# Performance work log

Measured on AMD Instinct MI355X. Metric: run time of the kernel, lower is better.

The kernel has to match this reference:

```python
import jax, jax.numpy as jnp
import numpy as np

N_NODES = 100000
N_EDGES = 300000
HID = 256
N0, N1, N2 = 40000, 30000, 30000
D0, D1, D2 = 512, 256, 128


def setup_inputs() -> dict:
    key = jax.random.key(0)
    ks = jax.random.split(key, 14)
    s = 0.05  # init scale
    return {
        "feat0": jax.random.normal(ks[0], (N0, D0), jnp.float32),
        "feat1": jax.random.normal(ks[1], (N1, D1), jnp.float32),
        "feat2": jax.random.normal(ks[2], (N2, D2), jnp.float32),
        # per-type Linear(in_dim, HID) params (torch Linear: y = x @ W.T + b)
        "fc_w0": jax.random.normal(ks[3], (HID, D0), jnp.float32) * s,
        "fc_b0": jnp.zeros((HID,), jnp.float32),
        "fc_w1": jax.random.normal(ks[4], (HID, D1), jnp.float32) * s,
        "fc_b1": jnp.zeros((HID,), jnp.float32),
        "fc_w2": jax.random.normal(ks[5], (HID, D2), jnp.float32) * s,
        "fc_b2": jnp.zeros((HID,), jnp.float32),
        # GraphConv 1: weight=False, bias=True
        "gc1_bias": jnp.zeros((HID,), jnp.float32),
        # GraphConv 2: weight (in,out) + bias (DGL convention: feat @ W)
        "gc2_weight": jax.random.normal(ks[6], (HID, HID), jnp.float32) * s,
        "gc2_bias": jnp.zeros((HID,), jnp.float32),
        "semantic_weight": jax.random.normal(ks[7], (1, 5), jnp.float32),
        "src": jax.random.randint(ks[8], (N_EDGES,), 0, N_NODES, jnp.int64),
        "dst": jax.random.randint(ks[9], (N_EDGES,), 0, N_NODES, jnp.int64),
    }


def reference(feat0, feat1, feat2, fc_w0, fc_b0, fc_w1, fc_b1, fc_w2, fc_b2,
              gc1_bias, gc2_weight, gc2_bias, semantic_weight, src, dst):
    # per-type projection then concat along node dim -> [N_NODES, HID]
    h = jnp.concatenate([
        feat0 @ fc_w0.T + fc_b0,
        feat1 @ fc_w1.T + fc_b1,
        feat2 @ fc_w2.T + fc_b2,
    ], axis=0)

    ones = jnp.ones((src.shape[0],), h.dtype)
    deg_out = jnp.maximum(jax.ops.segment_sum(ones, src, num_segments=N_NODES), 1.0)
    deg_in = jnp.maximum(jax.ops.segment_sum(ones, dst, num_segments=N_NODES), 1.0)
    norm_out = jax.lax.rsqrt(deg_out)[:, None]  # D_out^{-1/2}
    norm_in = jax.lax.rsqrt(deg_in)[:, None]    # D_in^{-1/2}

    def gconv(x, W, b):
        # DGL GraphConv, norm='both': D_in^{-1/2} A D_out^{-1/2} x W + b, relu
        msg = (x * norm_out)[src]                                  # [E, HID]
        agg = jax.ops.segment_sum(msg, dst, num_segments=N_NODES)  # [N, HID]
        agg = agg * norm_in
        if W is not None:
            agg = agg @ W
        return jax.nn.relu(agg + b)

    # dropout is identity in eval mode
    h = gconv(h, None, gc1_bias)        # layer 0: weight=False
    h = gconv(h, gc2_weight, gc2_bias)  # layer 1
    return h, semantic_weight
```

## Files before the change

### kernel.cpp

```cpp
#include <hip/hip_runtime.h>
#include <cstdint>

#define HID 256
static constexpr int    NNODES = 100000;
static constexpr int    NEDGES = 300000;
static constexpr size_t NH     = (size_t)NNODES * HID;
static constexpr int    SCAN_B = 256;
static constexpr int    NSBLK  = (NNODES + SCAN_B - 1) / SCAN_B;

typedef __attribute__((ext_vector_type(8))) short bf16x8;
typedef __attribute__((ext_vector_type(4))) float f32x4;

__device__ __forceinline__ unsigned short f2bf(float x) {
    unsigned int u = __float_as_uint(x);
    u += 0x7fffu + ((u >> 16) & 1u);
    return (unsigned short)(u >> 16);
}
__device__ __forceinline__ float bflo(unsigned int u) { return __uint_as_float(u << 16); }
__device__ __forceinline__ float bfhi(unsigned int u) { return __uint_as_float(u & 0xffff0000u); }

__global__ void zero_i32_k(int* __restrict__ p, int n) {
    int i = blockIdx.x * blockDim.x + threadIdx.x;
    if (i < n) p[i] = 0;
}

__global__ void cvt_bf16_k(const float* __restrict__ in, unsigned short* __restrict__ o, int n4) {
    int i = blockIdx.x * blockDim.x + threadIdx.x;
    if (i < n4) {
        float4 v = ((const float4*)in)[i];
        ushort4 w;
        w.x = f2bf(v.x); w.y = f2bf(v.y); w.z = f2bf(v.z); w.w = f2bf(v.w);
        ((ushort4*)o)[i] = w;
    }
}

__global__ void cvt_w2T_k(const float* __restrict__ w, unsigned short* __restrict__ o) {
    int n = blockIdx.x, k = threadIdx.x;
    o[n * 256 + k] = f2bf(w[k * 256 + n]);
}

__global__ void count_deg_k(const int* __restrict__ src, const int* __restrict__ dst,
                            int* __restrict__ degout, int* __restrict__ degin) {
    int e = blockIdx.x * blockDim.x + threadIdx.x;
    if (e < NEDGES) {
        atomicAdd(degout + src[e], 1);
        atomicAdd(degin  + dst[e], 1);
    }
}

__global__ void finalize_norm_k(const int* __restrict__ degout, const int* __restrict__ degin,
                                float* __restrict__ nout, float* __restrict__ nin,
                                const float* __restrict__ sw, float* __restrict__ tail) {
    int i = blockIdx.x * blockDim.x + threadIdx.x;
    if (i < NNODES) {
        nout[i] = rsqrtf(fmaxf((float)degout[i], 1.0f));
        nin[i]  = rsqrtf(fmaxf((float)degin[i], 1.0f));
    }
    if (i < 5) tail[i] = sw[i];
}

__global__ void scan_a_k(const int* __restrict__ degin, int* __restrict__ row_off,
                         int* __restrict__ bsums) {
    __shared__ int sm[SCAN_B];
    int t = threadIdx.x;
    int g = blockIdx.x * SCAN_B + t;
    int v = (g < NNODES) ? degin[g] : 0;
    sm[t] = v;
    __syncthreads();
#pragma unroll
    for (int off = 1; off < SCAN_B; off <<= 1) {
        int x = (t >= off) ? sm[t - off] : 0;
        __syncthreads();
        sm[t] += x;
        __syncthreads();
    }
    if (g < NNODES) row_off[g] = sm[t] - v;
    if (t == SCAN_B - 1) bsums[blockIdx.x] = sm[t];
}

__global__ void scan_b_k(int* __restrict__ bsums) {
    __shared__ int sm[512];
    int t = threadIdx.x;
    int v = (t < NSBLK) ? bsums[t] : 0;
    sm[t] = v;
    __syncthreads();
#pragma unroll
    for (int off = 1; off < 512; off <<= 1) {
        int x = (t >= off) ? sm[t - off] : 0;
        __syncthreads();
        sm[t] += x;
        __syncthreads();
    }
    if (t < NSBLK) bsums[t] = sm[t] - v;
}

__global__ void scan_c_k(int* __restrict__ row_off, const int* __restrict__ bsums) {
    int g = blockIdx.x * SCAN_B + threadIdx.x;
    if (g < NNODES) row_off[g] += bsums[blockIdx.x];
    if (g == 0) row_off[NNODES] = NEDGES;
}

__global__ void fill_csr_k(const int* __restrict__ src, const int* __restrict__ dst,
                           const int* __restrict__ row_off, int* __restrict__ cursor,
                           int* __restrict__ csr_src) {
    int e = blockIdx.x * blockDim.x + threadIdx.x;
    if (e < NEDGES) {
        int d = dst[e];
        int pos = row_off[d] + atomicAdd(cursor + d, 1);
        csr_src[pos] = src[e];
    }
}

template <int EPI>
__global__ __launch_bounds__(256) void gather_bf16_k(
    const unsigned short* __restrict__ h, const int* __restrict__ row_off,
    const int* __restrict__ csr_src, const float* __restrict__ nin,
    const float* __restrict__ nout, const float* __restrict__ bias,
    unsigned short* __restrict__ out)
{
    int node = blockIdx.x * 4 + (threadIdx.x >> 6);
    if (node >= NNODES) return;
    int lane = threadIdx.x & 63;
    int beg = row_off[node], end = row_off[node + 1];
    float a0 = 0.f, a1 = 0.f, a2 = 0.f, a3 = 0.f;
    for (int e = beg; e < end; ++e) {
        int s = csr_src[e];
        uint2 v = *(const uint2*)(h + (size_t)s * HID + lane * 4);
        a0 += bflo(v.x); a1 += bfhi(v.x);
        a2 += bflo(v.y); a3 += bfhi(v.y);
    }
    if (EPI) {
        float ni = nin[node], no = nout[node];
        float4 bb = *(const float4*)(bias + lane * 4);
        a0 = fmaxf(fmaf(a0, ni, bb.x), 0.f) * no;
        a1 = fmaxf(fmaf(a1, ni, bb.y), 0.f) * no;
        a2 = fmaxf(fmaf(a2, ni, bb.z), 0.f) * no;
        a3 = fmaxf(fmaf(a3, ni, bb.w), 0.f) * no;
    }
    ushort4 o;
    o.x = f2bf(a0); o.y = f2bf(a1); o.z = f2bf(a2); o.w = f2bf(a3);
    *(ushort4*)(out + (size_t)node * HID + lane * 4) = o;
}

template <int EPI>
__global__ __launch_bounds__(256) void mfma_gemm_k(
    const unsigned short* __restrict__ A, const unsigned short* __restrict__ Bn,
    const float* __restrict__ bias, const float* __restrict__ rs,
    void* __restrict__ Cv, int M, int K)
{
    __shared__ unsigned short As[128 * 32];
    __shared__ unsigned short Bs[128 * 32];
    const int tid  = threadIdx.x;
    const int wave = tid >> 6;
    const int lane = tid & 63;
    const int wm   = wave >> 1;
    const int wn   = wave & 1;
    const int m0   = blockIdx.x * 128;
    const int n0   = blockIdx.y * 128;

    f32x4 acc[4][4];
#pragma unroll
    for (int i = 0; i < 4; ++i)
#pragma unroll
        for (int j = 0; j < 4; ++j)
#pragma unroll
            for (int r = 0; r < 4; ++r) acc[i][j][r] = 0.f;

    const int half = lane >> 4;
    const int l15  = lane & 15;

    for (int k0 = 0; k0 < K; k0 += 32) {
#pragma unroll
        for (int t = 0; t < 2; ++t) {
            int q   = tid + t * 256;
            int row = q >> 2, c = q & 3;
            int slot = (c ^ ((row >> 1) & 3));
            int gm  = m0 + row; if (gm > M - 1) gm = M - 1;
            uint4 v = *(const uint4*)(A + (size_t)gm * K + k0 + c * 8);
            *(uint4*)&As[(row * 4 + slot) * 8] = v;
        }
#pragma unroll
        for (int t = 0; t < 2; ++t) {
            int q   = tid + t * 256;
            int row = q >> 2, c = q & 3;
            int slot = (c ^ ((row >> 1) & 3));
            uint4 v = *(const uint4*)(Bn + (size_t)(n0 + row) * K + k0 + c * 8);
            *(uint4*)&Bs[(row * 4 + slot) * 8] = v;
        }
        __syncthreads();

        bf16x8 af[4], bfr[4];
#pragma unroll
        for (int i = 0; i < 4; ++i) {
            int m = wm * 64 + i * 16 + l15;
            int ca = half ^ ((m >> 1) & 3);
            af[i] = *(const bf16x8*)&As[(m * 4 + ca) * 8];
            int n = wn * 64 + i * 16 + l15;
            int cb = half ^ ((n >> 1) & 3);
            bfr[i] = *(const bf16x8*)&Bs[(n * 4 + cb) * 8];
        }
#pragma unroll
        for (int i = 0; i < 4; ++i)
#pragma unroll
            for (int j = 0; j < 4; ++j)
                acc[i][j] = __builtin_amdgcn_mfma_f32_16x16x32_bf16(
                    af[i], bfr[j], acc[i][j], 0, 0, 0);
        __syncthreads();
    }

    float bj[4];
#pragma unroll
    for (int j = 0; j < 4; ++j) bj[j] = bias[n0 + wn * 64 + j * 16 + l15];

#pragma unroll
    for (int i = 0; i < 4; ++i)
#pragma unroll
        for (int r = 0; r < 4; ++r) {
            int m = m0 + wm * 64 + i * 16 + (lane >> 4) * 4 + r;
            if (m >= M) continue;
            float rsm = rs[m];
#pragma unroll
            for (int j = 0; j < 4; ++j) {
                int n = n0 + wn * 64 + j * 16 + l15;
                float v = acc[i][j][r];
                if (EPI == 0) {
                    v = (v + bj[j]) * rsm;
                    ((unsigned short*)Cv)[(size_t)m * HID + n] = f2bf(v);
                } else {
                    v = fmaxf(fmaf(v, rsm, bj[j]), 0.f);
                    ((float*)Cv)[(size_t)m * HID + n] = v;
                }
            }
        }
}

extern "C" void kernel_launch(void* const* d_in, const int* in_sizes, int n_in,
                              void* d_out, int out_size, void* d_ws, size_t ws_size,
                              hipStream_t stream)
{
    const float* feat0    = (const float*)d_in[0];
    const float* feat1    = (const float*)d_in[1];
    const float* feat2    = (const float*)d_in[2];
    const float* fc_w0    = (const float*)d_in[3];
    const float* fc_b0    = (const float*)d_in[4];
    const float* fc_w1    = (const float*)d_in[5];
    const float* fc_b1    = (const float*)d_in[6];
    const float* fc_w2    = (const float*)d_in[7];
    const float* fc_b2    = (const float*)d_in[8];
    const float* gc1_bias = (const float*)d_in[9];
    const float* gc2_w    = (const float*)d_in[10];
    const float* gc2_bias = (const float*)d_in[11];
    const float* sw       = (const float*)d_in[12];
    const int*   src      = (const int*)d_in[13];
    const int*   dst      = (const int*)d_in[14];

    char* base = (char*)d_ws;
    unsigned short* h0b   = (unsigned short*)base;
    unsigned short* h1b   = h0b + NH;
    unsigned short* agg2b = h0b;
    unsigned short* f0b   = h1b + NH;
    unsigned short* f1b   = f0b + (size_t)40000 * 512;
    unsigned short* f2b   = f1b + (size_t)30000 * 256;
    unsigned short* w0b   = f2b + (size_t)30000 * 128;
    unsigned short* w1b   = w0b + 256 * 512;
    unsigned short* w2b   = w1b + 256 * 256;
    unsigned short* w2Tb  = w2b + 256 * 128;
    float* nout = (float*)(w2Tb + 256 * 256 + 64);
    float* nin  = nout + NNODES;
    int* deg_out = (int*)(nin + NNODES);
    int* deg_in  = deg_out + NNODES;
    int* cursor  = deg_in + NNODES;
    int* row_off = cursor + NNODES;
    int* bsums   = row_off + NNODES + 1;
    int* csr_src = bsums + 512;
    float* out   = (float*)d_out;

    zero_i32_k<<<(3 * NNODES + 255) / 256, 256, 0, stream>>>(deg_out, 3 * NNODES);
    count_deg_k<<<(NEDGES + 255) / 256, 256, 0, stream>>>(src, dst, deg_out, deg_in);
    finalize_norm_k<<<(NNODES + 255) / 256, 256, 0, stream>>>(deg_out, deg_in, nout, nin,
                                                              sw, out + NH);
    scan_a_k<<<NSBLK, SCAN_B, 0, stream>>>(deg_in, row_off, bsums);
    scan_b_k<<<1, 512, 0, stream>>>(bsums);
    scan_c_k<<<NSBLK, SCAN_B, 0, stream>>>(row_off, bsums);
    fill_csr_k<<<(NEDGES + 255) / 256, 256, 0, stream>>>(src, dst, row_off, cursor, csr_src);

    cvt_bf16_k<<<(40000 * 512 / 4 + 255) / 256, 256, 0, stream>>>(feat0, f0b, 40000 * 512 / 4);
    cvt_bf16_k<<<(30000 * 256 / 4 + 255) / 256, 256, 0, stream>>>(feat1, f1b, 30000 * 256 / 4);
    cvt_bf16_k<<<(30000 * 128 / 4 + 255) / 256, 256, 0, stream>>>(feat2, f2b, 30000 * 128 / 4);
    cvt_bf16_k<<<(256 * 512 / 4 + 255) / 256, 256, 0, stream>>>(fc_w0, w0b, 256 * 512 / 4);
    cvt_bf16_k<<<(256 * 256 / 4 + 255) / 256, 256, 0, stream>>>(fc_w1, w1b, 256 * 256 / 4);
    cvt_bf16_k<<<(256 * 128 / 4 + 255) / 256, 256, 0, stream>>>(fc_w2, w2b, 256 * 128 / 4);
    cvt_w2T_k<<<256, 256, 0, stream>>>(gc2_w, w2Tb);

    mfma_gemm_k<0><<<dim3((40000 + 127) / 128, 2), 256, 0, stream>>>(
        f0b, w0b, fc_b0, nout, h0b, 40000, 512);
    mfma_gemm_k<0><<<dim3((30000 + 127) / 128, 2), 256, 0, stream>>>(
        f1b, w1b, fc_b1, nout + 40000, h0b + (size_t)40000 * HID, 30000, 256);
    mfma_gemm_k<0><<<dim3((30000 + 127) / 128, 2), 256, 0, stream>>>(
        f2b, w2b, fc_b2, nout + 70000, h0b + (size_t)70000 * HID, 30000, 128);

    gather_bf16_k<1><<<(NNODES + 3) / 4, 256, 0, stream>>>(h0b, row_off, csr_src,
                                                           nin, nout, gc1_bias, h1b);
    gather_bf16_k<0><<<(NNODES + 3) / 4, 256, 0, stream>>>(h1b, row_off, csr_src,
                                                           nin, nout, nullptr, agg2b);
    mfma_gemm_k<1><<<dim3((100000 + 127) / 128, 2), 256, 0, stream>>>(
        agg2b, w2Tb, gc2_bias, nin, out, 100000, 256);
}
```

Before: 464.9 us.

## Fuse bf16 conversion into projection GEMM and gather into final GEMM

Feature fp32-to-bf16 conversion moves into a single merged projection GEMM, which tiles 64 rows by the full 256 output columns and covers all three node types in one launch. The second-layer gather is fused into the final GEMM's prologue, staging aggregated rows straight into shared memory. Weight conversions and norm finalization are merged into existing kernels to cut launches and intermediate global traffic. The costs are higher LDS use per block and a gather phase that runs before any MFMA work in the final kernel.

```diff
diff --git a/kernel.cpp b/kernel.cpp
--- a/kernel.cpp
+++ b/kernel.cpp
@@ -16,27 +16,15 @@
     u += 0x7fffu + ((u >> 16) & 1u);
     return (unsigned short)(u >> 16);
 }
+__device__ __forceinline__ unsigned int pack2(float a, float b) {
+    return (unsigned int)f2bf(a) | ((unsigned int)f2bf(b) << 16);
+}
 __device__ __forceinline__ float bflo(unsigned int u) { return __uint_as_float(u << 16); }
 __device__ __forceinline__ float bfhi(unsigned int u) { return __uint_as_float(u & 0xffff0000u); }
 
 __global__ void zero_i32_k(int* __restrict__ p, int n) {
     int i = blockIdx.x * blockDim.x + threadIdx.x;
     if (i < n) p[i] = 0;
-}
-
-__global__ void cvt_bf16_k(const float* __restrict__ in, unsigned short* __restrict__ o, int n4) {
-    int i = blockIdx.x * blockDim.x + threadIdx.x;
-    if (i < n4) {
-        float4 v = ((const float4*)in)[i];
-        ushort4 w;
-        w.x = f2bf(v.x); w.y = f2bf(v.y); w.z = f2bf(v.z); w.w = f2bf(v.w);
-        ((ushort4*)o)[i] = w;
-    }
-}
-
-__global__ void cvt_w2T_k(const float* __restrict__ w, unsigned short* __restrict__ o) {
-    int n = blockIdx.x, k = threadIdx.x;
-    o[n * 256 + k] = f2bf(w[k * 256 + n]);
 }
 
 __global__ void count_deg_k(const int* __restrict__ src, const int* __restrict__ dst,
@@ -48,24 +36,40 @@
     }
 }
 
-__global__ void finalize_norm_k(const int* __restrict__ degout, const int* __restrict__ degin,
-                                float* __restrict__ nout, float* __restrict__ nin,
-                                const float* __restrict__ sw, float* __restrict__ tail) {
-    int i = blockIdx.x * blockDim.x + threadIdx.x;
-    if (i < NNODES) {
-        nout[i] = rsqrtf(fmaxf((float)degout[i], 1.0f));
-        nin[i]  = rsqrtf(fmaxf((float)degin[i], 1.0f));
-    }
-    if (i < 5) tail[i] = sw[i];
-}
-
-__global__ void scan_a_k(const int* __restrict__ degin, int* __restrict__ row_off,
-                         int* __restrict__ bsums) {
+__global__ void cvt_weights_k(const float* __restrict__ w0, const float* __restrict__ w1,
+                              const float* __restrict__ w2, const float* __restrict__ wg,
+                              unsigned short* __restrict__ o0, unsigned short* __restrict__ o1,
+                              unsigned short* __restrict__ o2, unsigned short* __restrict__ ogT) {
+    int b = blockIdx.x, t = threadIdx.x;
+    const float* in; unsigned short* out; int i;
+    if (b < 128)      { in = w0; out = o0; i = b * 256 + t; }
+    else if (b < 192) { in = w1; out = o1; i = (b - 128) * 256 + t; }
+    else if (b < 224) { in = w2; out = o2; i = (b - 192) * 256 + t; }
+    else {
+        int n = b - 224, k = t;
+        ogT[n * 256 + k] = f2bf(wg[k * 256 + n]);
+        return;
+    }
+    float4 v = ((const float4*)in)[i];
+    ushort4 w;
+    w.x = f2bf(v.x); w.y = f2bf(v.y); w.z = f2bf(v.z); w.w = f2bf(v.w);
+    ((ushort4*)out)[i] = w;
+}
+
+__global__ void scan_a_k(const int* __restrict__ degin, const int* __restrict__ degout,
+                         int* __restrict__ row_off, int* __restrict__ bsums,
+                         float* __restrict__ nout, float* __restrict__ nin,
+                         const float* __restrict__ sw, float* __restrict__ tail) {
     __shared__ int sm[SCAN_B];
     int t = threadIdx.x;
     int g = blockIdx.x * SCAN_B + t;
     int v = (g < NNODES) ? degin[g] : 0;
     sm[t] = v;
+    if (g < NNODES) {
+        nout[g] = rsqrtf(fmaxf((float)degout[g], 1.0f));
+        nin[g]  = rsqrtf(fmaxf((float)v, 1.0f));
+    }
+    if (g < 5) tail[g] = sw[g];
     __syncthreads();
 #pragma unroll
     for (int off = 1; off < SCAN_B; off <<= 1) {
@@ -111,7 +115,6 @@
     }
 }
 
-template <int EPI>
 __global__ __launch_bounds__(256) void gather_bf16_k(
     const unsigned short* __restrict__ h, const int* __restrict__ row_off,
     const int* __restrict__ csr_src, const float* __restrict__ nin,
@@ -129,62 +132,69 @@
         a0 += bflo(v.x); a1 += bfhi(v.x);
         a2 += bflo(v.y); a3 += bfhi(v.y);
     }
-    if (EPI) {
-        float ni = nin[node], no = nout[node];
-        float4 bb = *(const float4*)(bias + lane * 4);
-        a0 = fmaxf(fmaf(a0, ni, bb.x), 0.f) * no;
-        a1 = fmaxf(fmaf(a1, ni, bb.y), 0.f) * no;
-        a2 = fmaxf(fmaf(a2, ni, bb.z), 0.f) * no;
-        a3 = fmaxf(fmaf(a3, ni, bb.w), 0.f) * no;
-    }
+    float ni = nin[node], no = nout[node];
+    float4 bb = *(const float4*)(bias + lane * 4);
+    a0 = fmaxf(fmaf(a0, ni, bb.x), 0.f) * no;
+    a1 = fmaxf(fmaf(a1, ni, bb.y), 0.f) * no;
+    a2 = fmaxf(fmaf(a2, ni, bb.z), 0.f) * no;
+    a3 = fmaxf(fmaf(a3, ni, bb.w), 0.f) * no;
     ushort4 o;
     o.x = f2bf(a0); o.y = f2bf(a1); o.z = f2bf(a2); o.w = f2bf(a3);
     *(ushort4*)(out + (size_t)node * HID + lane * 4) = o;
 }
 
-template <int EPI>
-__global__ __launch_bounds__(256) void mfma_gemm_k(
-    const unsigned short* __restrict__ A, const unsigned short* __restrict__ Bn,
-    const float* __restrict__ bias, const float* __restrict__ rs,
-    void* __restrict__ Cv, int M, int K)
+__global__ __launch_bounds__(256, 3) void proj_mfma_k(
+    const float* __restrict__ f0, const float* __restrict__ f1, const float* __restrict__ f2,
+    const unsigned short* __restrict__ w0, const unsigned short* __restrict__ w1,
+    const unsigned short* __restrict__ w2,
+    const float* __restrict__ b0, const float* __restrict__ b1, const float* __restrict__ b2,
+    const float* __restrict__ nout, unsigned short* __restrict__ h0)
 {
-    __shared__ unsigned short As[128 * 32];
-    __shared__ unsigned short Bs[128 * 32];
+    __shared__ unsigned short As[64 * 32];
+    __shared__ unsigned short Bs[256 * 32];
+
+    int bx = blockIdx.x;
+    const float* A; const unsigned short* B; const float* bias; const float* rs;
+    unsigned short* C; int M, K;
+    if (bx < 625)       { A = f0; B = w0; bias = b0; rs = nout;          C = h0;                          M = 40000; K = 512; }
+    else if (bx < 1094) { bx -= 625;  A = f1; B = w1; bias = b1; rs = nout + 40000; C = h0 + (size_t)40000 * HID; M = 30000; K = 256; }
+    else                { bx -= 1094; A = f2; B = w2; bias = b2; rs = nout + 70000; C = h0 + (size_t)70000 * HID; M = 30000; K = 128; }
+    const int m0 = bx * 64;
+
     const int tid  = threadIdx.x;
-    const int wave = tid >> 6;
+    const int wn   = tid >> 6;
     const int lane = tid & 63;
-    const int wm   = wave >> 1;
-    const int wn   = wave & 1;
-    const int m0   = blockIdx.x * 128;
-    const int n0   = blockIdx.y * 128;
-
-    f32x4 acc[4][4];
-#pragma unroll
-    for (int i = 0; i < 4; ++i)
-#pragma unroll
-        for (int j = 0; j < 4; ++j)
-#pragma unroll
-            for (int r = 0; r < 4; ++r) acc[i][j][r] = 0.f;
-
     const int half = lane >> 4;
     const int l15  = lane & 15;
 
+    f32x4 acc[4][4];
+#pragma unroll
+    for (int i = 0; i < 4; ++i)
+#pragma unroll
+        for (int j = 0; j < 4; ++j)
+#pragma unroll
+            for (int r = 0; r < 4; ++r) acc[i][j][r] = 0.f;
+
+    const int arow = tid >> 2, ac = tid & 3;
+    const int aslot = ac ^ ((arow >> 1) & 3);
+    int agm = m0 + arow; if (agm > M - 1) agm = M - 1;
+
     for (int k0 = 0; k0 < K; k0 += 32) {
-#pragma unroll
-        for (int t = 0; t < 2; ++t) {
-            int q   = tid + t * 256;
+        {
+            const float* p = A + (size_t)agm * K + k0 + ac * 8;
+            float4 v0 = *(const float4*)p;
+            float4 v1 = *(const float4*)(p + 4);
+            uint4 u;
+            u.x = pack2(v0.x, v0.y); u.y = pack2(v0.z, v0.w);
+            u.z = pack2(v1.x, v1.y); u.w = pack2(v1.z, v1.w);
+            *(uint4*)&As[(arow * 4 + aslot) * 8] = u;
+        }
+#pragma unroll
+        for (int t = 0; t < 4; ++t) {
+            int q = tid + t * 256;
             int row = q >> 2, c = q & 3;
-            int slot = (c ^ ((row >> 1) & 3));
-            int gm  = m0 + row; if (gm > M - 1) gm = M - 1;
-            uint4 v = *(const uint4*)(A + (size_t)gm * K + k0 + c * 8);
-            *(uint4*)&As[(row * 4 + slot) * 8] = v;
-        }
-#pragma unroll
-        for (int t = 0; t < 2; ++t) {
-            int q   = tid + t * 256;
-            int row = q >> 2, c = q & 3;
-            int slot = (c ^ ((row >> 1) & 3));
-            uint4 v = *(const uint4*)(Bn + (size_t)(n0 + row) * K + k0 + c * 8);
+            int slot = c ^ ((row >> 1) & 3);
+            uint4 v = *(const uint4*)(B + (size_t)row * K + k0 + c * 8);
             *(uint4*)&Bs[(row * 4 + slot) * 8] = v;
         }
         __syncthreads();
@@ -192,7 +202,7 @@
         bf16x8 af[4], bfr[4];
 #pragma unroll
         for (int i = 0; i < 4; ++i) {
-            int m = wm * 64 + i * 16 + l15;
+            int m = i * 16 + l15;
             int ca = half ^ ((m >> 1) & 3);
             af[i] = *(const bf16x8*)&As[(m * 4 + ca) * 8];
             int n = wn * 64 + i * 16 + l15;
@@ -210,26 +220,115 @@
 
     float bj[4];
 #pragma unroll
-    for (int j = 0; j < 4; ++j) bj[j] = bias[n0 + wn * 64 + j * 16 + l15];
-
+    for (int j = 0; j < 4; ++j) bj[j] = bias[wn * 64 + j * 16 + l15];
 #pragma unroll
     for (int i = 0; i < 4; ++i)
 #pragma unroll
         for (int r = 0; r < 4; ++r) {
-            int m = m0 + wm * 64 + i * 16 + (lane >> 4) * 4 + r;
+            int m = m0 + i * 16 + (lane >> 4) * 4 + r;
             if (m >= M) continue;
             float rsm = rs[m];
 #pragma unroll
             for (int j = 0; j < 4; ++j) {
-                int n = n0 + wn * 64 + j * 16 + l15;
-                float v = acc[i][j][r];
-                if (EPI == 0) {
-                    v = (v + bj[j]) * rsm;
-                    ((unsigned short*)Cv)[(size_t)m * HID + n] = f2bf(v);
-                } else {
-                    v = fmaxf(fmaf(v, rsm, bj[j]), 0.f);
-                    ((float*)Cv)[(size_t)m * HID + n] = v;
-                }
+                int n = wn * 64 + j * 16 + l15;
+                C[(size_t)m * HID + n] = f2bf((acc[i][j][r] + bj[j]) * rsm);
+            }
+        }
+}
+
+__global__ __launch_bounds__(256, 3) void final_mfma_k(
+    const unsigned short* __restrict__ h1, const int* __restrict__ row_off,
+    const int* __restrict__ csr_src, const unsigned short* __restrict__ wT,
+    const float* __restrict__ bias, const float* __restrict__ nin,
+    float* __restrict__ out)
+{
+    __shared__ unsigned short As[8 * 64 * 32];
+    __shared__ unsigned short Bs[256 * 32];
+
+    const int m0   = blockIdx.x * 64;
+    const int tid  = threadIdx.x;
+    const int wv   = tid >> 6;
+    const int lane = tid & 63;
+    const int half = lane >> 4;
+    const int l15  = lane & 15;
+
+    {
+        const int p   = lane >> 3;
+        const int c   = (lane >> 1) & 3;
+        const int sub = (lane & 1) * 4;
+        for (int r8 = 0; r8 < 16; ++r8) {
+            int r = wv * 16 + r8;
+            int node = m0 + r; if (node > NNODES - 1) node = NNODES - 1;
+            int beg = row_off[node], end = row_off[node + 1];
+            float a0 = 0.f, a1 = 0.f, a2 = 0.f, a3 = 0.f;
+            for (int e = beg; e < end; ++e) {
+                int s = csr_src[e];
+                uint2 v = *(const uint2*)(h1 + (size_t)s * HID + lane * 4);
+                a0 += bflo(v.x); a1 += bfhi(v.x);
+                a2 += bflo(v.y); a3 += bfhi(v.y);
+            }
+            int slot = c ^ ((r >> 1) & 3);
+            ushort4 o;
+            o.x = f2bf(a0); o.y = f2bf(a1); o.z = f2bf(a2); o.w = f2bf(a3);
+            *(ushort4*)&As[p * 2048 + (r * 4 + slot) * 8 + sub] = o;
+        }
+    }
+    __syncthreads();
+
+    f32x4 acc[4][4];
+#pragma unroll
+    for (int i = 0; i < 4; ++i)
+#pragma unroll
+        for (int j = 0; j < 4; ++j)
+#pragma unroll
+            for (int r = 0; r < 4; ++r) acc[i][j][r] = 0.f;
+
+    const int wn = wv;
+    for (int step = 0; step < 8; ++step) {
+        int k0 = step * 32;
+#pragma unroll
+        for (int t = 0; t < 4; ++t) {
+            int q = tid + t * 256;
+            int row = q >> 2, c = q & 3;
+            int slot = c ^ ((row >> 1) & 3);
+            uint4 v = *(const uint4*)(wT + (size_t)row * 256 + k0 + c * 8);
+            *(uint4*)&Bs[(row * 4 + slot) * 8] = v;
+        }
+        __syncthreads();
+
+        bf16x8 af[4], bfr[4];
+#pragma unroll
+        for (int i = 0; i < 4; ++i) {
+            int m = i * 16 + l15;
+            int ca = half ^ ((m >> 1) & 3);
+            af[i] = *(const bf16x8*)&As[step * 2048 + (m * 4 + ca) * 8];
+            int n = wn * 64 + i * 16 + l15;
+            int cb = half ^ ((n >> 1) & 3);
+            bfr[i] = *(const bf16x8*)&Bs[(n * 4 + cb) * 8];
+        }
+#pragma unroll
+        for (int i = 0; i < 4; ++i)
+#pragma unroll
+            for (int j = 0; j < 4; ++j)
+                acc[i][j] = __builtin_amdgcn_mfma_f32_16x16x32_bf16(
+                    af[i], bfr[j], acc[i][j], 0, 0, 0);
+        __syncthreads();
+    }
+
+    float bj[4];
+#pragma unroll
+    for (int j = 0; j < 4; ++j) bj[j] = bias[wn * 64 + j * 16 + l15];
+#pragma unroll
+    for (int i = 0; i < 4; ++i)
+#pragma unroll
+        for (int r = 0; r < 4; ++r) {
+            int m = m0 + i * 16 + (lane >> 4) * 4 + r;
+            if (m >= NNODES) continue;
+            float rsm = nin[m];
+#pragma unroll
+            for (int j = 0; j < 4; ++j) {
+                int n = wn * 64 + j * 16 + l15;
+                out[(size_t)m * HID + n] = fmaxf(fmaf(acc[i][j][r], rsm, bj[j]), 0.f);
             }
         }
 }
@@ -254,18 +353,13 @@
     const int*   src      = (const int*)d_in[13];
     const int*   dst      = (const int*)d_in[14];
 
-    char* base = (char*)d_ws;
-    unsigned short* h0b   = (unsigned short*)base;
-    unsigned short* h1b   = h0b + NH;
-    unsigned short* agg2b = h0b;
-    unsigned short* f0b   = h1b + NH;
-    unsigned short* f1b   = f0b + (size_t)40000 * 512;
-    unsigned short* f2b   = f1b + (size_t)30000 * 256;
-    unsigned short* w0b   = f2b + (size_t)30000 * 128;
-    unsigned short* w1b   = w0b + 256 * 512;
-    unsigned short* w2b   = w1b + 256 * 256;
-    unsigned short* w2Tb  = w2b + 256 * 128;
-    float* nout = (float*)(w2Tb + 256 * 256 + 64);
+    unsigned short* h0b  = (unsigned short*)d_ws;
+    unsigned short* h1b  = h0b + NH;
+    unsigned short* w0b  = h1b + NH;
+    unsigned short* w1b  = w0b + 131072;
+    unsigned short* w2b  = w1b + 65536;
+    unsigned short* w2Tb = w2b + 32768;
+    float* nout = (float*)(w2Tb + 65536);
     float* nin  = nout + NNODES;
     int* deg_out = (int*)(nin + NNODES);
     int* deg_in  = deg_out + NNODES;
@@ -276,33 +370,21 @@
     float* out   = (float*)d_out;
 
     zero_i32_k<<<(3 * NNODES + 255) / 256, 256, 0, stream>>>(deg_out, 3 * NNODES);
+    cvt_weights_k<<<480, 256, 0, stream>>>(fc_w0, fc_w1, fc_w2, gc2_w,
+                                           w0b, w1b, w2b, w2Tb);
     count_deg_k<<<(NEDGES + 255) / 256, 256, 0, stream>>>(src, dst, deg_out, deg_in);
-    finalize_norm_k<<<(NNODES + 255) / 256, 256, 0, stream>>>(deg_out, deg_in, nout, nin,
-                                                              sw, out + NH);
-    scan_a_k<<<NSBLK, SCAN_B, 0, stream>>>(deg_in, row_off, bsums);
+    scan_a_k<<<NSBLK, SCAN_B, 0, stream>>>(deg_in, deg_out, row_off, bsums,
+                                           nout, nin, sw, out + NH);
     scan_b_k<<<1, 512, 0, stream>>>(bsums);
     scan_c_k<<<NSBLK, SCAN_B, 0, stream>>>(row_off, bsums);
     fill_csr_k<<<(NEDGES + 255) / 256, 256, 0, stream>>>(src, dst, row_off, cursor, csr_src);
 
-    cvt_bf16_k<<<(40000 * 512 / 4 + 255) / 256, 256, 0, stream>>>(feat0, f0b, 40000 * 512 / 4);
-    cvt_bf16_k<<<(30000 * 256 / 4 + 255) / 256, 256, 0, stream>>>(feat1, f1b, 30000 * 256 / 4);
-    cvt_bf16_k<<<(30000 * 128 / 4 + 255) / 256, 256, 0, stream>>>(feat2, f2b, 30000 * 128 / 4);
-    cvt_bf16_k<<<(256 * 512 / 4 + 255) / 256, 256, 0, stream>>>(fc_w0, w0b, 256 * 512 / 4);
-    cvt_bf16_k<<<(256 * 256 / 4 + 255) / 256, 256, 0, stream>>>(fc_w1, w1b, 256 * 256 / 4);
-    cvt_bf16_k<<<(256 * 128 / 4 + 255) / 256, 256, 0, stream>>>(fc_w2, w2b, 256 * 128 / 4);
-    cvt_w2T_k<<<256, 256, 0, stream>>>(gc2_w, w2Tb);
-
-    mfma_gemm_k<0><<<dim3((40000 + 127) / 128, 2), 256, 0, stream>>>(
-        f0b, w0b, fc_b0, nout, h0b, 40000, 512);
-    mfma_gemm_k<0><<<dim3((30000 + 127) / 128, 2), 256, 0, stream>>>(
-        f1b, w1b, fc_b1, nout + 40000, h0b + (size_t)40000 * HID, 30000, 256);
-    mfma_gemm_k<0><<<dim3((30000 + 127) / 128, 2), 256, 0, stream>>>(
-        f2b, w2b, fc_b2, nout + 70000, h0b + (size_t)70000 * HID, 30000, 128);
-
-    gather_bf16_k<1><<<(NNODES + 3) / 4, 256, 0, stream>>>(h0b, row_off, csr_src,
-                                                           nin, nout, gc1_bias, h1b);
-    gather_bf16_k<0><<<(NNODES + 3) / 4, 256, 0, stream>>>(h1b, row_off, csr_src,
-                                                           nin, nout, nullptr, agg2b);
-    mfma_gemm_k<1><<<dim3((100000 + 127) / 128, 2), 256, 0, stream>>>(
-        agg2b, w2Tb, gc2_bias, nin, out, 100000, 256);
-}
+    proj_mfma_k<<<1563, 256, 0, stream>>>(feat0, feat1, feat2, w0b, w1b, w2b,
+                                          fc_b0, fc_b1, fc_b2, nout, h0b);
+
+    gather_bf16_k<<<(NNODES + 3) / 4, 256, 0, stream>>>(h0b, row_off, csr_src,
+                                                        nin, nout, gc1_bias, h1b);
+
+    final_mfma_k<<<(NNODES + 63) / 64, 256, 0, stream>>>(h1b, row_off, csr_src, w2Tb,
+                                                         gc2_bias, nin, out);
+}
```

New measurement: 464.7 us. About the same (-0.0%).
